# Performance work log

Measured on AMD Instinct MI355X. Metric: run time of the kernel, lower is better.

Reference implementation:

```python
import jax, jax.numpy as jnp
import numpy as np

N_NODES = 50000
N_EDGES = 600000
D_IN = 128
D_HID = 128
N_CLASSES = 64
BN_EPS = 1e-5


def _bn(x, gamma, beta):
    # BatchNorm1d with batch statistics (training-mode math, biased var)
    mu = jnp.mean(x, axis=0)
    var = jnp.mean((x - mu) ** 2, axis=0)
    return gamma * (x - mu) * jax.lax.rsqrt(var + BN_EPS) + beta


def _gin_layer(h, src, dst, W1, b1, g1, be1, W2, b2, g2, be2):
    n = h.shape[0]
    msgs = h[src]  # [E, D] gather (copy_src)
    s = jax.ops.segment_sum(msgs, dst, num_segments=n)
    cnt = jax.ops.segment_sum(jnp.ones((dst.shape[0],), h.dtype), dst, num_segments=n)
    neigh = s / jnp.maximum(cnt, 1.0)[:, None]  # mean over in-neighbors, 0 if none
    x = h + neigh  # (1 + eps) * h + neigh with eps = 0
    x = jax.nn.relu(_bn(x @ W1 + b1, g1, be1))
    x = jax.nn.relu(_bn(x @ W2 + b2, g2, be2))
    return x


def setup_inputs() -> dict:
    key = jax.random.key(0)
    ks = jax.random.split(key, 32)
    inp = {
        "features": jax.random.normal(ks[0], (N_NODES, D_IN), dtype=jnp.float32),
        "src": jax.random.randint(ks[1], (N_EDGES,), 0, N_NODES, dtype=jnp.int32),
        "dst": jax.random.randint(ks[2], (N_EDGES,), 0, N_NODES, dtype=jnp.int32),
    }
    dims = [(D_IN, D_HID), (D_HID, D_HID), (D_HID, N_CLASSES)]
    ki = 3
    for li, (din, dout) in enumerate(dims):
        sc1 = 1.0 / np.sqrt(din)
        sc2 = 1.0 / np.sqrt(dout)
        inp[f"W1_{li}"] = jax.random.uniform(ks[ki + 0], (din, dout), jnp.float32, -sc1, sc1)
        inp[f"b1_{li}"] = jax.random.uniform(ks[ki + 1], (dout,), jnp.float32, -sc1, sc1)
        inp[f"g1_{li}"] = jnp.ones((dout,), jnp.float32)
        inp[f"be1_{li}"] = jnp.zeros((dout,), jnp.float32)
        inp[f"W2_{li}"] = jax.random.uniform(ks[ki + 2], (dout, dout), jnp.float32, -sc2, sc2)
        inp[f"b2_{li}"] = jax.random.uniform(ks[ki + 3], (dout,), jnp.float32, -sc2, sc2)
        inp[f"g2_{li}"] = jnp.ones((dout,), jnp.float32)
        inp[f"be2_{li}"] = jnp.zeros((dout,), jnp.float32)
        ki += 4
    return inp


def reference(features, src, dst,
              W1_0, b1_0, g1_0, be1_0, W2_0, b2_0, g2_0, be2_0,
              W1_1, b1_1, g1_1, be1_1, W2_1, b2_1, g2_1, be2_1,
              W1_2, b1_2, g1_2, be1_2, W2_2, b2_2, g2_2, be2_2):
    h = features
    h = _gin_layer(h, src, dst, W1_0, b1_0, g1_0, be1_0, W2_0, b2_0, g2_0, be2_0)
    h = _gin_layer(h, src, dst, W1_1, b1_1, g1_1, be1_1, W2_1, b2_1, g2_1, be2_1)
    h = _gin_layer(h, src, dst, W1_2, b1_2, g1_2, be1_2, W2_2, b2_2, g2_2, be2_2)
    return h
```

## Files before the change

### kernel.cpp

```cpp
#include <hip/hip_runtime.h>

#define NN 50000
#define NE 600000
#define SREP 32

typedef __attribute__((ext_vector_type(8))) short short8;
typedef __attribute__((ext_vector_type(4))) float f32x4;

__device__ __forceinline__ float bf2f(unsigned short u){
  union { unsigned int i; float f; } c; c.i = ((unsigned int)u) << 16; return c.f;
}
__device__ __forceinline__ float lof(unsigned v){
  union { unsigned int i; float f; } c; c.i = v << 16; return c.f;
}
__device__ __forceinline__ float hif(unsigned v){
  union { unsigned int i; float f; } c; c.i = v & 0xFFFF0000u; return c.f;
}
__device__ __forceinline__ unsigned short f2b(float f){
  union { float f; unsigned int i; } c; c.f = f;
  unsigned int i = c.i;
  return (unsigned short)((i + 0x7FFFu + ((i >> 16) & 1u)) >> 16);
}

template<int N>
__device__ __forceinline__ void compute_ab(const float* __restrict__ st,
    const float* __restrict__ gam, const float* __restrict__ bet, float2* absh){
  int tid = threadIdx.x;
  if (tid < N){
    float s = 0.f, q = 0.f;
    #pragma unroll
    for (int r = 0; r < SREP; ++r){
      s += st[r*2*N + tid];
      q += st[r*2*N + N + tid];
    }
    float mu = s * (1.f/(float)NN);
    float var = fmaxf(q * (1.f/(float)NN) - mu*mu, 0.f);
    float a = gam[tid] * rsqrtf(var + 1e-5f);
    absh[tid] = make_float2(a, bet[tid] - mu*a);
  }
}

struct W6 { const float* w[6]; unsigned short* o[6]; };
__global__ __launch_bounds__(256) void k_pre(const float* __restrict__ features,
    unsigned short* __restrict__ H0, unsigned short* __restrict__ X,
    unsigned short* __restrict__ Y1, unsigned short* __restrict__ Y2,
    const int* __restrict__ dst, int* __restrict__ deg, W6 jb){
  int b = blockIdx.x, tid = threadIdx.x;
  if (b < 6250){
    int i = b*256 + tid;
    float4 v = ((const float4*)features)[i];
    uint2 o;
    o.x = (unsigned)f2b(v.x) | ((unsigned)f2b(v.y) << 16);
    o.y = (unsigned)f2b(v.z) | ((unsigned)f2b(v.w) << 16);
    ((uint2*)H0)[i] = o;
  } else if (b < 6250 + 2344){
    int i = (b - 6250)*256 + tid;
    if (i < NE) atomicAdd(&deg[dst[i]], 1);
  } else if (b < 6250 + 2344 + 304){
    int i = (b - 8594)*256 + tid;
    if (i < 77824){
      int job, base, K, N;
      if (i < 65536){ job = i >> 14; base = job << 14; K = 128; N = 128; }
      else if (i < 73728){ job = 4; base = 65536; K = 128; N = 64; }
      else { job = 5; base = 73728; K = 64; N = 64; }
      int t = i - base;
      int k = t & (K-1);
      int n = t / K;
      jb.o[job][t] = f2b(jb.w[job][k*N + n]);
    }
  } else {
    if (tid < 64){
      unsigned short* bufs[4] = {H0, X, Y1, Y2};
      unsigned short* bp = bufs[tid >> 4];
      ((uint4*)bp)[(size_t)NN*16 + (tid & 15)] = make_uint4(0,0,0,0);
    }
  }
}

__global__ void k_offsets(const int* __restrict__ deg, int* __restrict__ row_off,
                          int* __restrict__ cur, int* __restrict__ col,
                          int* __restrict__ total){
  __shared__ int ws[4];
  __shared__ int wbase[4];
  int tid = threadIdx.x, lane = tid & 63, wid = tid >> 6;
  int i = blockIdx.x*256 + tid;
  int v = (i < NN) ? deg[i] : 0;
  int vp = (v + 3) & ~3;
  int x = vp;
  #pragma unroll
  for (int o = 1; o < 64; o <<= 1){
    int t = __shfl_up(x, o);
    if (lane >= o) x += t;
  }
  if (lane == 63) ws[wid] = x;
  __syncthreads();
  if (tid == 0){
    int s0 = ws[0], s1 = ws[1], s2 = ws[2], s3 = ws[3];
    int b = atomicAdd(total, s0+s1+s2+s3);
    wbase[0] = b; wbase[1] = b+s0; wbase[2] = b+s0+s1; wbase[3] = b+s0+s1+s2;
  }
  __syncthreads();
  if (i < NN){
    int excl = wbase[wid] + x - vp;
    row_off[i] = excl;
    cur[i] = excl;
    for (int t = v; t < vp; ++t) col[excl + t] = NN;
  }
}

__global__ void k_fill(const int* __restrict__ src, const int* __restrict__ dst,
                       int* __restrict__ cur, int* __restrict__ col, int e){
  int i = blockIdx.x*blockDim.x + threadIdx.x;
  if (i >= e) return;
  int d = dst[i];
  int pos = atomicAdd(&cur[d], 1);
  col[pos] = src[i];
}

template<bool APPLY>
__global__ __launch_bounds__(256) void k_agg(const unsigned short* __restrict__ H,
    const float* __restrict__ st, const float* __restrict__ gam,
    const float* __restrict__ bet, const int* __restrict__ row_off,
    const int* __restrict__ deg, const int* __restrict__ col,
    unsigned short* __restrict__ X){
  __shared__ float2 absh[128];
  if (APPLY){ compute_ab<128>(st, gam, bet, absh); __syncthreads(); }
  int lane = threadIdx.x & 63;
  int wave = threadIdx.x >> 6;
  int half = lane >> 5, hl = lane & 31;
  int p = hl & 15, qq = hl >> 4;
  float ac[8], bc[8];
  if (APPLY){
    #pragma unroll
    for (int e = 0; e < 8; ++e){ float2 t = absh[p*8 + e]; ac[e] = t.x; bc[e] = t.y; }
  }
  const uint4* hp4 = (const uint4*)H;
  int P = blockIdx.x*4 + wave;
  int node = 2*P + half;
  int beg = row_off[node];
  int d = deg[node];
  int dp = (d + 3) & ~3;
  float s[8];
  #pragma unroll
  for (int e = 0; e < 8; ++e) s[e] = 0.f;
  auto ACC = [&](uint4 v){
    float x;
    x = lof(v.x); if (APPLY) x = fmaxf(fmaf(x,ac[0],bc[0]),0.f); s[0] += x;
    x = hif(v.x); if (APPLY) x = fmaxf(fmaf(x,ac[1],bc[1]),0.f); s[1] += x;
    x = lof(v.y); if (APPLY) x = fmaxf(fmaf(x,ac[2],bc[2]),0.f); s[2] += x;
    x = hif(v.y); if (APPLY) x = fmaxf(fmaf(x,ac[3],bc[3]),0.f); s[3] += x;
    x = lof(v.z); if (APPLY) x = fmaxf(fmaf(x,ac[4],bc[4]),0.f); s[4] += x;
    x = hif(v.z); if (APPLY) x = fmaxf(fmaf(x,ac[5],bc[5]),0.f); s[5] += x;
    x = lof(v.w); if (APPLY) x = fmaxf(fmaf(x,ac[6],bc[6]),0.f); s[6] += x;
    x = hif(v.w); if (APPLY) x = fmaxf(fmaf(x,ac[7],bc[7]),0.f); s[7] += x;
  };
  for (int base = 0; base < dp; base += 32){
    int wdp = dp - base; if (wdp > 32) wdp = 32;
    int cvs = (hl < wdp) ? col[beg + base + hl] : NN;
    int steps = wdp >> 1;
    for (int s0 = 0; s0 < steps; s0 += 4){
      int idx[4], val[4];
      #pragma unroll
      for (int u = 0; u < 4; ++u){
        int stp = s0 + u;
        int v = (stp < steps);
        int e = v ? (2*stp + qq) : 0;
        int ix = __shfl(cvs, 32*half + e);
        idx[u] = v ? ix : NN;
        val[u] = v;
      }
      uint4 vv[4];
      #pragma unroll
      for (int u = 0; u < 4; ++u) vv[u] = hp4[(size_t)idx[u]*16 + p];
      #pragma unroll
      for (int u = 0; u < 4; ++u) if (val[u]) ACC(vv[u]);
    }
  }
  #pragma unroll
  for (int e = 0; e < 8; ++e) s[e] += __shfl_xor(s[e], 16);
  if (qq == 0){
    uint4 hv = hp4[(size_t)node*16 + p];
    float inv = 1.f / (float)(d > 0 ? d : 1);
    float npad = (float)(dp - d);
    float h[8] = {lof(hv.x),hif(hv.x),lof(hv.y),hif(hv.y),
                  lof(hv.z),hif(hv.z),lof(hv.w),hif(hv.w)};
    unsigned w[4];
    #pragma unroll
    for (int u = 0; u < 4; ++u){
      float x0 = h[2*u], x1 = h[2*u+1];
      float s0 = s[2*u], s1 = s[2*u+1];
      if (APPLY){
        x0 = fmaxf(fmaf(x0,ac[2*u],bc[2*u]),0.f);
        x1 = fmaxf(fmaf(x1,ac[2*u+1],bc[2*u+1]),0.f);
        s0 -= npad * fmaxf(bc[2*u], 0.f);
        s1 -= npad * fmaxf(bc[2*u+1], 0.f);
      }
      x0 += s0*inv;
      x1 += s1*inv;
      w[u] = (unsigned)f2b(x0) | ((unsigned)f2b(x1) << 16);
    }
    ((uint4*)X)[(size_t)node*16 + p] = make_uint4(w[0], w[1], w[2], w[3]);
  }
}

template<int KSTEPS, int NT, int CS, bool APPLY>
__global__ __launch_bounds__(512) void k_gemm(const unsigned short* __restrict__ A,
    const unsigned short* __restrict__ BT,
    const float* __restrict__ stIn, const float* __restrict__ gam,
    const float* __restrict__ bet,
    unsigned short* __restrict__ Y, float* __restrict__ statsAcc){
  constexpr int K = KSTEPS*32;
  constexpr int N = CS*NT*16;
  constexpr int TILES = NN/16;
  constexpr int TPB = (CS==2) ? 4 : 8;
  __shared__ float red[2*N];
  __shared__ float2 absh[K];
  if (APPLY) compute_ab<K>(stIn, gam, bet, absh);
  int tid = threadIdx.x;
  int lane = tid & 63, w = tid >> 6;
  int r = lane & 15, g = lane >> 4;
  int tile = blockIdx.x*TPB + ((CS==2) ? (w & 3) : w);
  int ch = (CS==2) ? (w >> 2) : 0;
  bool valid = (tile < TILES);
  int arow = valid ? tile*16 + r : 0;
  short8 af[KSTEPS];
  #pragma unroll
  for (int kk = 0; kk < KSTEPS; ++kk)
    af[kk] = *(const short8*)(A + (size_t)arow*K + kk*32 + g*8);
  short8 bf[KSTEPS][NT];
  #pragma unroll
  for (int kk = 0; kk < KSTEPS; ++kk)
    #pragma unroll
    for (int t = 0; t < NT; ++t)
      bf[kk][t] = *(const short8*)(BT + (size_t)(ch*NT*16 + t*16 + r)*K + kk*32 + g*8);
  for (int i = tid; i < 2*N; i += 512) red[i] = 0.f;
  __syncthreads();
  if (APPLY){
    #pragma unroll
    for (int kk = 0; kk < KSTEPS; ++kk){
      #pragma unroll
      for (int j = 0; j < 8; ++j){
        float2 pab = absh[kk*32 + g*8 + j];
        float v = fmaxf(fmaf(bf2f((unsigned short)af[kk][j]), pab.x, pab.y), 0.f);
        af[kk][j] = (short)f2b(v);
      }
    }
  }
  f32x4 acc[NT];
  #pragma unroll
  for (int t = 0; t < NT; ++t) acc[t] = (f32x4){0.f,0.f,0.f,0.f};
  #pragma unroll
  for (int kk = 0; kk < KSTEPS; ++kk)
    #pragma unroll
    for (int t = 0; t < NT; ++t)
      acc[t] = __builtin_amdgcn_mfma_f32_16x16x32_bf16(af[kk], bf[kk][t], acc[t], 0, 0, 0);
  if (valid){
    #pragma unroll
    for (int t = 0; t < NT; ++t){
      int c = ch*NT*16 + t*16 + r;
      float ys = 0.f, yq = 0.f;
      #pragma unroll
      for (int j = 0; j < 4; ++j){
        float y = acc[t][j];
        Y[(size_t)(tile*16 + g*4 + j)*N + c] = (unsigned short)f2b(y);
        ys += y; yq += y*y;
      }
      ys += __shfl_xor(ys, 16); ys += __shfl_xor(ys, 32);
      yq += __shfl_xor(yq, 16); yq += __shfl_xor(yq, 32);
      if (g == 0){
        atomicAdd(&red[c], ys);
        atomicAdd(&red[N+c], yq);
      }
    }
  }
  __syncthreads();
  float* dstAcc = statsAcc + (size_t)(blockIdx.x & (SREP-1)) * (2*N);
  for (int i = tid; i < 2*N; i += 512) atomicAdd(&dstAcc[i], red[i]);
}

__global__ __launch_bounds__(256) void k_final(const unsigned short* __restrict__ Y,
    const float* __restrict__ st, const float* __restrict__ gam,
    const float* __restrict__ bet, float* __restrict__ out){
  __shared__ float2 absh[64];
  compute_ab<64>(st, gam, bet, absh);
  __syncthreads();
  for (int i = blockIdx.x*256 + threadIdx.x; i < NN*32; i += gridDim.x*256){
    unsigned v = ((const unsigned*)Y)[i];
    int c = (i & 31)*2;
    float2 p0 = absh[c], p1 = absh[c+1];
    float o0 = fmaxf(fmaf(lof(v), p0.x, p0.y), 0.f);
    float o1 = fmaxf(fmaf(hif(v), p1.x, p1.y), 0.f);
    ((float2*)out)[i] = make_float2(o0, o1);
  }
}

extern "C" void kernel_launch(void* const* d_in, const int* in_sizes, int n_in,
                              void* d_out, int out_size, void* d_ws, size_t ws_size,
                              hipStream_t stream) {
  const float* features = (const float*)d_in[0];
  const int* src = (const int*)d_in[1];
  const int* dst = (const int*)d_in[2];
  const float *Wp[6], *gp[6], *bep[6];
  for (int l = 0; l < 3; ++l){
    int base = 3 + 8*l;
    Wp[2*l]    = (const float*)d_in[base+0];
    gp[2*l]    = (const float*)d_in[base+2];
    bep[2*l]   = (const float*)d_in[base+3];
    Wp[2*l+1]  = (const float*)d_in[base+4];
    gp[2*l+1]  = (const float*)d_in[base+6];
    bep[2*l+1] = (const float*)d_in[base+7];
  }

  size_t off = 0;
  char* base = (char*)d_ws;
  auto carve = [&](size_t bytes)->char* {
    char* q = base + off; off += (bytes + 255) & ~(size_t)255; return q;
  };
  int* deg   = (int*)carve((size_t)NN*4);
  int* total = (int*)carve(4);
  float* stats[6];
  for (int i = 0; i < 6; ++i) stats[i] = (float*)carve((size_t)SREP*256*4);
  size_t zbytes = (size_t)(base + off - (char*)deg);

  int* row_off = (int*)carve((size_t)NN*4);
  int* cur     = (int*)carve((size_t)NN*4);
  int* col     = (int*)carve((size_t)(NE + 3*NN)*4);
  unsigned short* wt[6];
  for (int i = 0; i < 6; ++i) wt[i] = (unsigned short*)carve(128*128*2);
  unsigned short* H0 = (unsigned short*)carve((size_t)(NN+1)*128*2);
  unsigned short* X  = (unsigned short*)carve((size_t)(NN+1)*128*2);
  unsigned short* Y1 = (unsigned short*)carve((size_t)(NN+1)*128*2);
  unsigned short* Y2 = (unsigned short*)carve((size_t)(NN+1)*128*2);

  hipMemsetAsync(deg, 0, zbytes, stream);

  W6 jb;
  for (int i = 0; i < 6; ++i){ jb.w[i] = Wp[i]; jb.o[i] = wt[i]; }
  k_pre<<<8899, 256, 0, stream>>>(features, H0, X, Y1, Y2, dst, deg, jb);
  k_offsets<<<(NN+255)/256, 256, 0, stream>>>(deg, row_off, cur, col, total);
  k_fill<<<(NE+255)/256, 256, 0, stream>>>(src, dst, cur, col, NE);

  const int agg_grid = 6250;

  k_agg<false><<<agg_grid, 256, 0, stream>>>(H0, nullptr, nullptr, nullptr, row_off, deg, col, X);
  k_gemm<4,4,2,false><<<782, 512, 0, stream>>>(X, wt[0], nullptr, nullptr, nullptr, Y1, stats[0]);
  k_gemm<4,4,2,true ><<<782, 512, 0, stream>>>(Y1, wt[1], stats[0], gp[0], bep[0], Y2, stats[1]);
  k_agg<true ><<<agg_grid, 256, 0, stream>>>(Y2, stats[1], gp[1], bep[1], row_off, deg, col, X);
  k_gemm<4,4,2,false><<<782, 512, 0, stream>>>(X, wt[2], nullptr, nullptr, nullptr, Y1, stats[2]);
  k_gemm<4,4,2,true ><<<782, 512, 0, stream>>>(Y1, wt[3], stats[2], gp[2], bep[2], Y2, stats[3]);
  k_agg<true ><<<agg_grid, 256, 0, stream>>>(Y2, stats[3], gp[3], bep[3], row_off, deg, col, X);
  k_gemm<4,4,1,false><<<391, 512, 0, stream>>>(X, wt[4], nullptr, nullptr, nullptr, Y1, stats[4]);
  k_gemm<2,4,1,true ><<<391, 512, 0, stream>>>(Y1, wt[5], stats[4], gp[4], bep[4], Y2, stats[5]);
  k_final<<<782, 256, 0, stream>>>(Y2, stats[5], gp[5], bep[5], (float*)d_out);
}
```

Measured before the change: 290.0 us.

## Fuse neighbor aggregation with first GEMM via LDS tile, widen stats replication

Merges the aggregation kernel with the following W1 GEMM. Each 512-thread block aggregates 16 nodes into a swizzled LDS tile and then runs MFMA directly on it, so the X intermediate buffer and its global round trip disappear. BN statistics partial buffers are widened (128 or 64 replicas) to reduce atomic contention, at the cost of longer reductions in compute_ab. The fused kernel uses only NT_ALL waves for the GEMM phase and issues many small blocks, which may leave waves idle and add per-block stat atomics.

Measured after the change: 294.3 us. No clear change (+1.5%).

```diff
diff --git a/kernel.cpp b/kernel.cpp
--- a/kernel.cpp
+++ b/kernel.cpp
@@ -2,7 +2,6 @@
 
 #define NN 50000
 #define NE 600000
-#define SREP 32
 
 typedef __attribute__((ext_vector_type(8))) short short8;
 typedef __attribute__((ext_vector_type(4))) float f32x4;
@@ -22,14 +21,14 @@
   return (unsigned short)((i + 0x7FFFu + ((i >> 16) & 1u)) >> 16);
 }
 
-template<int N>
+template<int N, int SR>
 __device__ __forceinline__ void compute_ab(const float* __restrict__ st,
     const float* __restrict__ gam, const float* __restrict__ bet, float2* absh){
   int tid = threadIdx.x;
   if (tid < N){
     float s = 0.f, q = 0.f;
-    #pragma unroll
-    for (int r = 0; r < SREP; ++r){
+    #pragma unroll 16
+    for (int r = 0; r < SR; ++r){
       s += st[r*2*N + tid];
       q += st[r*2*N + N + tid];
     }
@@ -42,8 +41,7 @@
 
 struct W6 { const float* w[6]; unsigned short* o[6]; };
 __global__ __launch_bounds__(256) void k_pre(const float* __restrict__ features,
-    unsigned short* __restrict__ H0, unsigned short* __restrict__ X,
-    unsigned short* __restrict__ Y1, unsigned short* __restrict__ Y2,
+    unsigned short* __restrict__ H0, unsigned short* __restrict__ Y2,
     const int* __restrict__ dst, int* __restrict__ deg, W6 jb){
   int b = blockIdx.x, tid = threadIdx.x;
   if (b < 6250){
@@ -69,9 +67,8 @@
       jb.o[job][t] = f2b(jb.w[job][k*N + n]);
     }
   } else {
-    if (tid < 64){
-      unsigned short* bufs[4] = {H0, X, Y1, Y2};
-      unsigned short* bp = bufs[tid >> 4];
+    if (tid < 32){
+      unsigned short* bp = (tid < 16) ? H0 : Y2;
       ((uint4*)bp)[(size_t)NN*16 + (tid & 15)] = make_uint4(0,0,0,0);
     }
   }
@@ -117,16 +114,25 @@
   col[pos] = src[i];
 }
 
-template<bool APPLY>
-__global__ __launch_bounds__(256) void k_agg(const unsigned short* __restrict__ H,
-    const float* __restrict__ st, const float* __restrict__ gam,
-    const float* __restrict__ bet, const int* __restrict__ row_off,
-    const int* __restrict__ deg, const int* __restrict__ col,
-    unsigned short* __restrict__ X){
+template<int NT_ALL, bool APPLY, int SRIN, int SROUT>
+__global__ __launch_bounds__(512) void k_fused(const unsigned short* __restrict__ H,
+    const unsigned short* __restrict__ BT,
+    const float* __restrict__ stIn, const float* __restrict__ gam,
+    const float* __restrict__ bet,
+    const int* __restrict__ row_off, const int* __restrict__ deg,
+    const int* __restrict__ col,
+    unsigned short* __restrict__ Y, float* __restrict__ statsAcc){
+  constexpr int K = 128;
+  constexpr int N = NT_ALL*16;
   __shared__ float2 absh[128];
-  if (APPLY){ compute_ab<128>(st, gam, bet, absh); __syncthreads(); }
-  int lane = threadIdx.x & 63;
-  int wave = threadIdx.x >> 6;
+  __shared__ unsigned short As[16*128];
+  __shared__ float red[2*N];
+  int tid = threadIdx.x;
+  if (APPLY) compute_ab<128, SRIN>(stIn, gam, bet, absh);
+  for (int i = tid; i < 2*N; i += 512) red[i] = 0.f;
+  if (APPLY) __syncthreads();
+
+  int lane = tid & 63, wave = tid >> 6;
   int half = lane >> 5, hl = lane & 31;
   int p = hl & 15, qq = hl >> 4;
   float ac[8], bc[8];
@@ -135,8 +141,8 @@
     for (int e = 0; e < 8; ++e){ float2 t = absh[p*8 + e]; ac[e] = t.x; bc[e] = t.y; }
   }
   const uint4* hp4 = (const uint4*)H;
-  int P = blockIdx.x*4 + wave;
-  int node = 2*P + half;
+  int t16 = 2*wave + half;
+  int node = blockIdx.x*16 + t16;
   int beg = row_off[node];
   int d = deg[node];
   int dp = (d + 3) & ~3;
@@ -199,11 +205,46 @@
       x1 += s1*inv;
       w[u] = (unsigned)f2b(x0) | ((unsigned)f2b(x1) << 16);
     }
-    ((uint4*)X)[(size_t)node*16 + p] = make_uint4(w[0], w[1], w[2], w[3]);
-  }
-}
-
-template<int KSTEPS, int NT, int CS, bool APPLY>
+    int slot = p ^ (t16 & 7);
+    ((uint4*)As)[t16*16 + slot] = make_uint4(w[0], w[1], w[2], w[3]);
+  }
+  __syncthreads();
+
+  int r = lane & 15, g = lane >> 4;
+  if (wave < NT_ALL){
+    short8 af[4];
+    #pragma unroll
+    for (int kk = 0; kk < 4; ++kk)
+      af[kk] = *(const short8*)(As + r*128 + (((4*kk + g) ^ (r & 7)) * 8));
+    short8 bfr[4];
+    #pragma unroll
+    for (int kk = 0; kk < 4; ++kk)
+      bfr[kk] = *(const short8*)(BT + (size_t)(wave*16 + r)*K + kk*32 + g*8);
+    f32x4 acc = (f32x4){0.f,0.f,0.f,0.f};
+    #pragma unroll
+    for (int kk = 0; kk < 4; ++kk)
+      acc = __builtin_amdgcn_mfma_f32_16x16x32_bf16(af[kk], bfr[kk], acc, 0, 0, 0);
+    int c = wave*16 + r;
+    float ys = 0.f, yq = 0.f;
+    #pragma unroll
+    for (int j = 0; j < 4; ++j){
+      float y = acc[j];
+      Y[(size_t)(blockIdx.x*16 + g*4 + j)*N + c] = (unsigned short)f2b(y);
+      ys += y; yq += y*y;
+    }
+    ys += __shfl_xor(ys, 16); ys += __shfl_xor(ys, 32);
+    yq += __shfl_xor(yq, 16); yq += __shfl_xor(yq, 32);
+    if (g == 0){
+      atomicAdd(&red[c], ys);
+      atomicAdd(&red[N+c], yq);
+    }
+  }
+  __syncthreads();
+  float* dstAcc = statsAcc + (size_t)(blockIdx.x & (SROUT-1)) * (2*N);
+  for (int i = tid; i < 2*N; i += 512) atomicAdd(&dstAcc[i], red[i]);
+}
+
+template<int KSTEPS, int NT, int CS, int SRIN, int SROUT>
 __global__ __launch_bounds__(512) void k_gemm(const unsigned short* __restrict__ A,
     const unsigned short* __restrict__ BT,
     const float* __restrict__ stIn, const float* __restrict__ gam,
@@ -215,7 +256,7 @@
   constexpr int TPB = (CS==2) ? 4 : 8;
   __shared__ float red[2*N];
   __shared__ float2 absh[K];
-  if (APPLY) compute_ab<K>(stIn, gam, bet, absh);
+  compute_ab<K, SRIN>(stIn, gam, bet, absh);
   int tid = threadIdx.x;
   int lane = tid & 63, w = tid >> 6;
   int r = lane & 15, g = lane >> 4;
@@ -235,15 +276,13 @@
       bf[kk][t] = *(const short8*)(BT + (size_t)(ch*NT*16 + t*16 + r)*K + kk*32 + g*8);
   for (int i = tid; i < 2*N; i += 512) red[i] = 0.f;
   __syncthreads();
-  if (APPLY){
-    #pragma unroll
-    for (int kk = 0; kk < KSTEPS; ++kk){
-      #pragma unroll
-      for (int j = 0; j < 8; ++j){
-        float2 pab = absh[kk*32 + g*8 + j];
-        float v = fmaxf(fmaf(bf2f((unsigned short)af[kk][j]), pab.x, pab.y), 0.f);
-        af[kk][j] = (short)f2b(v);
-      }
+  #pragma unroll
+  for (int kk = 0; kk < KSTEPS; ++kk){
+    #pragma unroll
+    for (int j = 0; j < 8; ++j){
+      float2 pab = absh[kk*32 + g*8 + j];
+      float v = fmaxf(fmaf(bf2f((unsigned short)af[kk][j]), pab.x, pab.y), 0.f);
+      af[kk][j] = (short)f2b(v);
     }
   }
   f32x4 acc[NT];
@@ -274,7 +313,7 @@
     }
   }
   __syncthreads();
-  float* dstAcc = statsAcc + (size_t)(blockIdx.x & (SREP-1)) * (2*N);
+  float* dstAcc = statsAcc + (size_t)(blockIdx.x & (SROUT-1)) * (2*N);
   for (int i = tid; i < 2*N; i += 512) atomicAdd(&dstAcc[i], red[i]);
 }
 
@@ -282,7 +321,7 @@
     const float* __restrict__ st, const float* __restrict__ gam,
     const float* __restrict__ bet, float* __restrict__ out){
   __shared__ float2 absh[64];
-  compute_ab<64>(st, gam, bet, absh);
+  compute_ab<64, 64>(st, gam, bet, absh);
   __syncthreads();
   for (int i = blockIdx.x*256 + threadIdx.x; i < NN*32; i += gridDim.x*256){
     unsigned v = ((const unsigned*)Y)[i];
@@ -319,7 +358,7 @@
   int* deg   = (int*)carve((size_t)NN*4);
   int* total = (int*)carve(4);
   float* stats[6];
-  for (int i = 0; i < 6; ++i) stats[i] = (float*)carve((size_t)SREP*256*4);
+  for (int i = 0; i < 6; ++i) stats[i] = (float*)carve((size_t)128*256*4);
   size_t zbytes = (size_t)(base + off - (char*)deg);
 
   int* row_off = (int*)carve((size_t)NN*4);
@@ -328,7 +367,6 @@
   unsigned short* wt[6];
   for (int i = 0; i < 6; ++i) wt[i] = (unsigned short*)carve(128*128*2);
   unsigned short* H0 = (unsigned short*)carve((size_t)(NN+1)*128*2);
-  unsigned short* X  = (unsigned short*)carve((size_t)(NN+1)*128*2);
   unsigned short* Y1 = (unsigned short*)carve((size_t)(NN+1)*128*2);
   unsigned short* Y2 = (unsigned short*)carve((size_t)(NN+1)*128*2);
 
@@ -336,20 +374,18 @@
 
   W6 jb;
   for (int i = 0; i < 6; ++i){ jb.w[i] = Wp[i]; jb.o[i] = wt[i]; }
-  k_pre<<<8899, 256, 0, stream>>>(features, H0, X, Y1, Y2, dst, deg, jb);
+  k_pre<<<8899, 256, 0, stream>>>(features, H0, Y2, dst, deg, jb);
   k_offsets<<<(NN+255)/256, 256, 0, stream>>>(deg, row_off, cur, col, total);
   k_fill<<<(NE+255)/256, 256, 0, stream>>>(src, dst, cur, col, NE);
 
-  const int agg_grid = 6250;
-
-  k_agg<false><<<agg_grid, 256, 0, stream>>>(H0, nullptr, nullptr, nullptr, row_off, deg, col, X);
-  k_gemm<4,4,2,false><<<782, 512, 0, stream>>>(X, wt[0], nullptr, nullptr, nullptr, Y1, stats[0]);
-  k_gemm<4,4,2,true ><<<782, 512, 0, stream>>>(Y1, wt[1], stats[0], gp[0], bep[0], Y2, stats[1]);
-  k_agg<true ><<<agg_grid, 256, 0, stream>>>(Y2, stats[1], gp[1], bep[1], row_off, deg, col, X);
-  k_gemm<4,4,2,false><<<782, 512, 0, stream>>>(X, wt[2], nullptr, nullptr, nullptr, Y1, stats[2]);
-  k_gemm<4,4,2,true ><<<782, 512, 0, stream>>>(Y1, wt[3], stats[2], gp[2], bep[2], Y2, stats[3]);
-  k_agg<true ><<<agg_grid, 256, 0, stream>>>(Y2, stats[3], gp[3], bep[3], row_off, deg, col, X);
-  k_gemm<4,4,1,false><<<391, 512, 0, stream>>>(X, wt[4], nullptr, nullptr, nullptr, Y1, stats[4]);
-  k_gemm<2,4,1,true ><<<391, 512, 0, stream>>>(Y1, wt[5], stats[4], gp[4], bep[4], Y2, stats[5]);
+  k_fused<8,false,64,128><<<3125, 512, 0, stream>>>(H0, wt[0], nullptr, nullptr, nullptr,
+      row_off, deg, col, Y1, stats[0]);
+  k_gemm<4,4,2,128,64><<<782, 512, 0, stream>>>(Y1, wt[1], stats[0], gp[0], bep[0], Y2, stats[1]);
+  k_fused<8,true,64,128><<<3125, 512, 0, stream>>>(Y2, wt[2], stats[1], gp[1], bep[1],
+      row_off, deg, col, Y1, stats[2]);
+  k_gemm<4,4,2,128,64><<<782, 512, 0, stream>>>(Y1, wt[3], stats[2], gp[2], bep[2], Y2, stats[3]);
+  k_fused<4,true,64,128><<<3125, 512, 0, stream>>>(Y2, wt[4], stats[3], gp[3], bep[3],
+      row_off, deg, col, Y1, stats[4]);
+  k_gemm<2,4,1,128,64><<<391, 512, 0, stream>>>(Y1, wt[5], stats[4], gp[4], bep[4], Y2, stats[5]);
   k_final<<<782, 256, 0, stream>>>(Y2, stats[5], gp[5], bep[5], (float*)d_out);
 }
```

## Unfuse BN-apply from aggregation into separate pass; widen gather unroll

Applied to the files above, without the earlier changes.

Moves the BatchNorm+ReLU application out of the aggregation inner loop into a separate elementwise pass that writes a normalized bf16 buffer. Aggregation then just sums gathered rows, unrolled 8-wide without per-edge validity masks, because the padding row is zero. The stats replication count is doubled to reduce atomic contention. In exchange it adds one extra full read and write of the node features per layer.

Measured after the change: 304.5 us. 5.0% more time.

```diff
diff --git a/kernel.cpp b/kernel.cpp
--- a/kernel.cpp
+++ b/kernel.cpp
@@ -2,7 +2,7 @@
 
 #define NN 50000
 #define NE 600000
-#define SREP 32
+#define SREP 64
 
 typedef __attribute__((ext_vector_type(8))) short short8;
 typedef __attribute__((ext_vector_type(4))) float f32x4;
@@ -28,7 +28,7 @@
   int tid = threadIdx.x;
   if (tid < N){
     float s = 0.f, q = 0.f;
-    #pragma unroll
+    #pragma unroll 16
     for (int r = 0; r < SREP; ++r){
       s += st[r*2*N + tid];
       q += st[r*2*N + N + tid];
@@ -42,8 +42,7 @@
 
 struct W6 { const float* w[6]; unsigned short* o[6]; };
 __global__ __launch_bounds__(256) void k_pre(const float* __restrict__ features,
-    unsigned short* __restrict__ H0, unsigned short* __restrict__ X,
-    unsigned short* __restrict__ Y1, unsigned short* __restrict__ Y2,
+    unsigned short* __restrict__ H0, unsigned short* __restrict__ Hp,
     const int* __restrict__ dst, int* __restrict__ deg, W6 jb){
   int b = blockIdx.x, tid = threadIdx.x;
   if (b < 6250){
@@ -69,9 +68,8 @@
       jb.o[job][t] = f2b(jb.w[job][k*N + n]);
     }
   } else {
-    if (tid < 64){
-      unsigned short* bufs[4] = {H0, X, Y1, Y2};
-      unsigned short* bp = bufs[tid >> 4];
+    if (tid < 32){
+      unsigned short* bp = (tid < 16) ? H0 : Hp;
       ((uint4*)bp)[(size_t)NN*16 + (tid & 15)] = make_uint4(0,0,0,0);
     }
   }
@@ -117,23 +115,13 @@
   col[pos] = src[i];
 }
 
-template<bool APPLY>
 __global__ __launch_bounds__(256) void k_agg(const unsigned short* __restrict__ H,
-    const float* __restrict__ st, const float* __restrict__ gam,
-    const float* __restrict__ bet, const int* __restrict__ row_off,
-    const int* __restrict__ deg, const int* __restrict__ col,
-    unsigned short* __restrict__ X){
-  __shared__ float2 absh[128];
-  if (APPLY){ compute_ab<128>(st, gam, bet, absh); __syncthreads(); }
+    const int* __restrict__ row_off, const int* __restrict__ deg,
+    const int* __restrict__ col, unsigned short* __restrict__ X){
   int lane = threadIdx.x & 63;
   int wave = threadIdx.x >> 6;
   int half = lane >> 5, hl = lane & 31;
   int p = hl & 15, qq = hl >> 4;
-  float ac[8], bc[8];
-  if (APPLY){
-    #pragma unroll
-    for (int e = 0; e < 8; ++e){ float2 t = absh[p*8 + e]; ac[e] = t.x; bc[e] = t.y; }
-  }
   const uint4* hp4 = (const uint4*)H;
   int P = blockIdx.x*4 + wave;
   int node = 2*P + half;
@@ -144,36 +132,29 @@
   #pragma unroll
   for (int e = 0; e < 8; ++e) s[e] = 0.f;
   auto ACC = [&](uint4 v){
-    float x;
-    x = lof(v.x); if (APPLY) x = fmaxf(fmaf(x,ac[0],bc[0]),0.f); s[0] += x;
-    x = hif(v.x); if (APPLY) x = fmaxf(fmaf(x,ac[1],bc[1]),0.f); s[1] += x;
-    x = lof(v.y); if (APPLY) x = fmaxf(fmaf(x,ac[2],bc[2]),0.f); s[2] += x;
-    x = hif(v.y); if (APPLY) x = fmaxf(fmaf(x,ac[3],bc[3]),0.f); s[3] += x;
-    x = lof(v.z); if (APPLY) x = fmaxf(fmaf(x,ac[4],bc[4]),0.f); s[4] += x;
-    x = hif(v.z); if (APPLY) x = fmaxf(fmaf(x,ac[5],bc[5]),0.f); s[5] += x;
-    x = lof(v.w); if (APPLY) x = fmaxf(fmaf(x,ac[6],bc[6]),0.f); s[6] += x;
-    x = hif(v.w); if (APPLY) x = fmaxf(fmaf(x,ac[7],bc[7]),0.f); s[7] += x;
+    s[0] += lof(v.x); s[1] += hif(v.x);
+    s[2] += lof(v.y); s[3] += hif(v.y);
+    s[4] += lof(v.z); s[5] += hif(v.z);
+    s[6] += lof(v.w); s[7] += hif(v.w);
   };
   for (int base = 0; base < dp; base += 32){
     int wdp = dp - base; if (wdp > 32) wdp = 32;
     int cvs = (hl < wdp) ? col[beg + base + hl] : NN;
     int steps = wdp >> 1;
-    for (int s0 = 0; s0 < steps; s0 += 4){
-      int idx[4], val[4];
-      #pragma unroll
-      for (int u = 0; u < 4; ++u){
+    for (int s0 = 0; s0 < steps; s0 += 8){
+      int idx[8];
+      #pragma unroll
+      for (int u = 0; u < 8; ++u){
         int stp = s0 + u;
-        int v = (stp < steps);
-        int e = v ? (2*stp + qq) : 0;
+        int e = (stp < steps) ? (2*stp + qq) : 0;
         int ix = __shfl(cvs, 32*half + e);
-        idx[u] = v ? ix : NN;
-        val[u] = v;
+        idx[u] = (stp < steps) ? ix : NN;
       }
-      uint4 vv[4];
-      #pragma unroll
-      for (int u = 0; u < 4; ++u) vv[u] = hp4[(size_t)idx[u]*16 + p];
-      #pragma unroll
-      for (int u = 0; u < 4; ++u) if (val[u]) ACC(vv[u]);
+      uint4 vv[8];
+      #pragma unroll
+      for (int u = 0; u < 8; ++u) vv[u] = hp4[(size_t)idx[u]*16 + p];
+      #pragma unroll
+      for (int u = 0; u < 8; ++u) ACC(vv[u]);
     }
   }
   #pragma unroll
@@ -181,22 +162,13 @@
   if (qq == 0){
     uint4 hv = hp4[(size_t)node*16 + p];
     float inv = 1.f / (float)(d > 0 ? d : 1);
-    float npad = (float)(dp - d);
     float h[8] = {lof(hv.x),hif(hv.x),lof(hv.y),hif(hv.y),
                   lof(hv.z),hif(hv.z),lof(hv.w),hif(hv.w)};
     unsigned w[4];
     #pragma unroll
     for (int u = 0; u < 4; ++u){
-      float x0 = h[2*u], x1 = h[2*u+1];
-      float s0 = s[2*u], s1 = s[2*u+1];
-      if (APPLY){
-        x0 = fmaxf(fmaf(x0,ac[2*u],bc[2*u]),0.f);
-        x1 = fmaxf(fmaf(x1,ac[2*u+1],bc[2*u+1]),0.f);
-        s0 -= npad * fmaxf(bc[2*u], 0.f);
-        s1 -= npad * fmaxf(bc[2*u+1], 0.f);
-      }
-      x0 += s0*inv;
-      x1 += s1*inv;
+      float x0 = h[2*u]   + s[2*u]*inv;
+      float x1 = h[2*u+1] + s[2*u+1]*inv;
       w[u] = (unsigned)f2b(x0) | ((unsigned)f2b(x1) << 16);
     }
     ((uint4*)X)[(size_t)node*16 + p] = make_uint4(w[0], w[1], w[2], w[3]);
@@ -278,6 +250,22 @@
   for (int i = tid; i < 2*N; i += 512) atomicAdd(&dstAcc[i], red[i]);
 }
 
+__global__ __launch_bounds__(256) void k_apply(const unsigned short* __restrict__ Y,
+    const float* __restrict__ st, const float* __restrict__ gam,
+    const float* __restrict__ bet, unsigned short* __restrict__ Hp){
+  __shared__ float2 absh[128];
+  compute_ab<128>(st, gam, bet, absh);
+  __syncthreads();
+  for (int i = blockIdx.x*256 + threadIdx.x; i < NN*64; i += gridDim.x*256){
+    unsigned v = ((const unsigned*)Y)[i];
+    int c = (i & 63)*2;
+    float2 p0 = absh[c], p1 = absh[c+1];
+    float o0 = fmaxf(fmaf(lof(v), p0.x, p0.y), 0.f);
+    float o1 = fmaxf(fmaf(hif(v), p1.x, p1.y), 0.f);
+    ((unsigned*)Hp)[i] = (unsigned)f2b(o0) | ((unsigned)f2b(o1) << 16);
+  }
+}
+
 __global__ __launch_bounds__(256) void k_final(const unsigned short* __restrict__ Y,
     const float* __restrict__ st, const float* __restrict__ gam,
     const float* __restrict__ bet, float* __restrict__ out){
@@ -328,27 +316,30 @@
   unsigned short* wt[6];
   for (int i = 0; i < 6; ++i) wt[i] = (unsigned short*)carve(128*128*2);
   unsigned short* H0 = (unsigned short*)carve((size_t)(NN+1)*128*2);
-  unsigned short* X  = (unsigned short*)carve((size_t)(NN+1)*128*2);
-  unsigned short* Y1 = (unsigned short*)carve((size_t)(NN+1)*128*2);
-  unsigned short* Y2 = (unsigned short*)carve((size_t)(NN+1)*128*2);
+  unsigned short* Hp = (unsigned short*)carve((size_t)(NN+1)*128*2);
+  unsigned short* X  = (unsigned short*)carve((size_t)NN*128*2);
+  unsigned short* Y1 = (unsigned short*)carve((size_t)NN*128*2);
+  unsigned short* Y2 = (unsigned short*)carve((size_t)NN*128*2);
 
   hipMemsetAsync(deg, 0, zbytes, stream);
 
   W6 jb;
   for (int i = 0; i < 6; ++i){ jb.w[i] = Wp[i]; jb.o[i] = wt[i]; }
-  k_pre<<<8899, 256, 0, stream>>>(features, H0, X, Y1, Y2, dst, deg, jb);
+  k_pre<<<8899, 256, 0, stream>>>(features, H0, Hp, dst, deg, jb);
   k_offsets<<<(NN+255)/256, 256, 0, stream>>>(deg, row_off, cur, col, total);
   k_fill<<<(NE+255)/256, 256, 0, stream>>>(src, dst, cur, col, NE);
 
   const int agg_grid = 6250;
 
-  k_agg<false><<<agg_grid, 256, 0, stream>>>(H0, nullptr, nullptr, nullptr, row_off, deg, col, X);
+  k_agg<<<agg_grid, 256, 0, stream>>>(H0, row_off, deg, col, X);
   k_gemm<4,4,2,false><<<782, 512, 0, stream>>>(X, wt[0], nullptr, nullptr, nullptr, Y1, stats[0]);
   k_gemm<4,4,2,true ><<<782, 512, 0, stream>>>(Y1, wt[1], stats[0], gp[0], bep[0], Y2, stats[1]);
-  k_agg<true ><<<agg_grid, 256, 0, stream>>>(Y2, stats[1], gp[1], bep[1], row_off, deg, col, X);
+  k_apply<<<1563, 256, 0, stream>>>(Y2, stats[1], gp[1], bep[1], Hp);
+  k_agg<<<agg_grid, 256, 0, stream>>>(Hp, row_off, deg, col, X);
   k_gemm<4,4,2,false><<<782, 512, 0, stream>>>(X, wt[2], nullptr, nullptr, nullptr, Y1, stats[2]);
   k_gemm<4,4,2,true ><<<782, 512, 0, stream>>>(Y1, wt[3], stats[2], gp[2], bep[2], Y2, stats[3]);
-  k_agg<true ><<<agg_grid, 256, 0, stream>>>(Y2, stats[3], gp[3], bep[3], row_off, deg, col, X);
+  k_apply<<<1563, 256, 0, stream>>>(Y2, stats[3], gp[3], bep[3], H0);
+  k_agg<<<agg_grid, 256, 0, stream>>>(H0, row_off, deg, col, X);
   k_gemm<4,4,1,false><<<391, 512, 0, stream>>>(X, wt[4], nullptr, nullptr, nullptr, Y1, stats[4]);
   k_gemm<2,4,1,true ><<<391, 512, 0, stream>>>(Y1, wt[5], stats[4], gp[4], bep[4], Y2, stats[5]);
   k_final<<<782, 256, 0, stream>>>(Y2, stats[5], gp[5], bep[5], (float*)d_out);
```
